# Optimization experiments

Measured on AMD Instinct MI355X. Metric: run time of the kernel, lower is better.

Reference implementation:

```python
import jax, jax.numpy as jnp
import numpy as np

D_MODEL = 1024
D_HIDDEN = 32   # per-head MPS bond dimension
N_HEADS = 8
D_FF = 4096
EPS_LN = 1e-5
EPS_NORM = 1e-6


def layernorm(x, g, b):
    m = jnp.mean(x, axis=-1, keepdims=True)
    v = jnp.mean(jnp.square(x - m), axis=-1, keepdims=True)
    return (x - m) * jax.lax.rsqrt(v + EPS_LN) * g + b


def mps_recurrence(x, Wa, ba, h0, Wo, bo):
    # x: [B,S,D]. Per-token per-head transfer matrices A_t in R^{dh x dh}.
    B, S, D = x.shape
    A = (x @ Wa + ba).reshape(B, S, N_HEADS, D_HIDDEN, D_HIDDEN)
    A = jnp.moveaxis(A, 1, 0)  # [S,B,H,dh,dh]
    h_init = jnp.broadcast_to(h0, (B, N_HEADS, D_HIDDEN))  # [B,H,dh]

    def step(h, A_t):
        h = jnp.einsum('bhij,bhj->bhi', A_t, h)
        h = h / (jnp.linalg.norm(h, axis=-1, keepdims=True) + EPS_NORM)
        return h, h

    _, ys = jax.lax.scan(step, h_init, A)          # ys: [S,B,H,dh]
    ys = jnp.moveaxis(ys, 0, 1).reshape(B, S, N_HEADS * D_HIDDEN)
    return ys @ Wo + bo                            # [B,S,D]


def setup_inputs() -> dict:
    key = jax.random.key(0)
    ks = jax.random.split(key, 12)
    B, S, D = 4, 2048, D_MODEL
    inv = 1.0 / np.sqrt(D)
    inv_hd = 1.0 / np.sqrt(N_HEADS * D_HIDDEN)
    return {
        'x': jax.random.normal(ks[0], (B, S, D), jnp.float32),
        'ln1_g': jnp.ones((D,), jnp.float32),
        'ln1_b': jnp.zeros((D,), jnp.float32),
        'Wa': jax.random.normal(ks[1], (D, N_HEADS * D_HIDDEN * D_HIDDEN), jnp.float32) * inv,
        'ba': jnp.zeros((N_HEADS * D_HIDDEN * D_HIDDEN,), jnp.float32),
        'h0': jax.random.normal(ks[2], (N_HEADS, D_HIDDEN), jnp.float32) / np.sqrt(D_HIDDEN),
        'Wo': jax.random.normal(ks[3], (N_HEADS * D_HIDDEN, D), jnp.float32) * inv_hd,
        'bo': jnp.zeros((D,), jnp.float32),
        'ln2_g': jnp.ones((D,), jnp.float32),
        'ln2_b': jnp.zeros((D,), jnp.float32),
        'W1': jax.random.normal(ks[4], (D, D_FF), jnp.float32) * inv,
        'b1': jnp.zeros((D_FF,), jnp.float32),
        'W2': jax.random.normal(ks[5], (D_FF, D), jnp.float32) / np.sqrt(D_FF),
        'b2': jnp.zeros((D,), jnp.float32),
    }


def reference(x, ln1_g, ln1_b, Wa, ba, h0, Wo, bo, ln2_g, ln2_b, W1, b1, W2, b2):
    # Dropout in eval mode (identity).
    x = x + mps_recurrence(layernorm(x, ln1_g, ln1_b), Wa, ba, h0, Wo, bo)
    h = layernorm(x, ln2_g, ln2_b)
    ffn = jax.nn.gelu(h @ W1 + b1, approximate=False) @ W2 + b2
    return x + ffn
```

## Files before the change

### kernel.cpp

```cpp
#include <hip/hip_runtime.h>
#include <hip/hip_bf16.h>
#include <math.h>

typedef float f32x4 __attribute__((ext_vector_type(4)));
typedef __bf16 bf16x4 __attribute__((ext_vector_type(4)));
typedef __bf16 bf16x8 __attribute__((ext_vector_type(8)));

#define AS1(p) ((const __attribute__((address_space(1))) void*)(p))
#define AS3(p) ((__attribute__((address_space(3))) void*)(p))

static constexpr int D_MODEL = 1024;
static constexpr int S_LEN   = 2048;
static constexpr int BATCH   = 4;
static constexpr int NTOK    = BATCH * S_LEN;
static constexpr int NH      = 8;
static constexpr int DH      = 32;
static constexpr int NA      = NH * DH * DH;
static constexpr int D_FF    = 4096;
static constexpr int CHUNK   = 16;
static constexpr int NCHUNK  = S_LEN / CHUNK;

__device__ __forceinline__ void xcd_swizzle(int& bx, int& by) {
  int gx = gridDim.x;
  int orig = by * gx + bx;
  int r8 = orig & 7, j = orig >> 3;
  int bxn = j % gx, grp = j / gx;
  bx = bxn;
  by = grp * 8 + r8;
}

__device__ __forceinline__ float gelu_erf_fast(float v) {
  float z = fabsf(v) * 0.70710678118654752f;
  float t = __builtin_amdgcn_rcpf(fmaf(0.3275911f, z, 1.0f));
  float p = t * (0.254829592f + t * (-0.284496736f + t * (1.421413741f +
            t * (-1.453152027f + t * 1.061405429f))));
  float e = __builtin_amdgcn_exp2f(-1.4426950408889634f * z * z);
  float er = 1.0f - p * e;
  er = (v < 0.0f) ? -er : er;
  return 0.5f * v * (1.0f + er);
}

__global__ __launch_bounds__(256) void transpose_bf16(
    const float* __restrict__ in, __bf16* __restrict__ out, int R, int C) {
  __shared__ float tile[32][33];
  int tx = threadIdx.x & 31, ty = threadIdx.x >> 5;
  int c0 = blockIdx.x * 32, r0 = blockIdx.y * 32;
  for (int i = ty; i < 32; i += 8)
    tile[i][tx] = in[(size_t)(r0 + i) * C + c0 + tx];
  __syncthreads();
  for (int i = ty; i < 32; i += 8)
    out[(size_t)(c0 + i) * R + r0 + tx] = (__bf16)tile[tx][i];
}

__global__ __launch_bounds__(256) void transpose_split(
    const float* __restrict__ in, __bf16* __restrict__ ohi,
    __bf16* __restrict__ olo, int R, int C) {
  __shared__ float tile[32][33];
  int tx = threadIdx.x & 31, ty = threadIdx.x >> 5;
  int c0 = blockIdx.x * 32, r0 = blockIdx.y * 32;
  for (int i = ty; i < 32; i += 8)
    tile[i][tx] = in[(size_t)(r0 + i) * C + c0 + tx];
  __syncthreads();
  for (int i = ty; i < 32; i += 8) {
    float v = tile[tx][i];
    __bf16 h = (__bf16)v;
    ohi[(size_t)(c0 + i) * R + r0 + tx] = h;
    olo[(size_t)(c0 + i) * R + r0 + tx] = (__bf16)(v - (float)h);
  }
}

template <int MODE>
__global__ __launch_bounds__(256) void ln_kernel(
    const float* __restrict__ in, const float* __restrict__ g,
    const float* __restrict__ bta, void* __restrict__ outv,
    void* __restrict__ outv2) {
  int row = blockIdx.x, tid = threadIdx.x;
  const float4* in4 = (const float4*)(in + (size_t)row * D_MODEL);
  float4 v = in4[tid];
  float s  = v.x + v.y + v.z + v.w;
  float ss = v.x * v.x + v.y * v.y + v.z * v.z + v.w * v.w;
  for (int o = 32; o; o >>= 1) { s += __shfl_down(s, o); ss += __shfl_down(ss, o); }
  __shared__ float ps[4], pq[4];
  int lane = tid & 63, w = tid >> 6;
  if (lane == 0) { ps[w] = s; pq[w] = ss; }
  __syncthreads();
  s  = ps[0] + ps[1] + ps[2] + ps[3];
  ss = pq[0] + pq[1] + pq[2] + pq[3];
  float mean = s * (1.0f / D_MODEL);
  float var  = ss * (1.0f / D_MODEL) - mean * mean;
  float inv  = rsqrtf(fmaxf(var, 0.0f) + 1e-5f);
  float4 gv = ((const float4*)g)[tid];
  float4 bv = ((const float4*)bta)[tid];
  float o0 = (v.x - mean) * inv * gv.x + bv.x;
  float o1 = (v.y - mean) * inv * gv.y + bv.y;
  float o2 = (v.z - mean) * inv * gv.z + bv.z;
  float o3 = (v.w - mean) * inv * gv.w + bv.w;
  if (MODE == 1) {
    float4 o = {o0, o1, o2, o3};
    ((float4*)outv)[(size_t)row * (D_MODEL / 4) + tid] = o;
  } else if (MODE == 0) {
    bf16x4 o;
    o[0] = (__bf16)o0; o[1] = (__bf16)o1; o[2] = (__bf16)o2; o[3] = (__bf16)o3;
    ((bf16x4*)outv)[(size_t)row * (D_MODEL / 4) + tid] = o;
  } else {
    bf16x4 oh, ol;
    oh[0] = (__bf16)o0; oh[1] = (__bf16)o1; oh[2] = (__bf16)o2; oh[3] = (__bf16)o3;
    ol[0] = (__bf16)(o0 - (float)oh[0]);
    ol[1] = (__bf16)(o1 - (float)oh[1]);
    ol[2] = (__bf16)(o2 - (float)oh[2]);
    ol[3] = (__bf16)(o3 - (float)oh[3]);
    ((bf16x4*)outv )[(size_t)row * (D_MODEL / 4) + tid] = oh;
    ((bf16x4*)outv2)[(size_t)row * (D_MODEL / 4) + tid] = ol;
  }
}

enum { EPI_BF16_BIAS = 0, EPI_BF16_BIAS_GELU = 1, EPI_F32_BIAS_RES = 2,
       EPI_F32_BIAS_ONLY = 3 };

#define PH_SYNC()                                      \
  do {                                                 \
    __builtin_amdgcn_sched_barrier(0);                 \
    __builtin_amdgcn_s_barrier();                      \
    __builtin_amdgcn_sched_barrier(0);                 \
  } while (0)
#define LGKM0()                                        \
  do {                                                 \
    asm volatile("s_waitcnt lgkmcnt(0)" ::: "memory"); \
    __builtin_amdgcn_sched_barrier(0);                 \
  } while (0)
#define GEMM8_QUAD(I0, J0)                                                   \
  do {                                                                       \
    __builtin_amdgcn_s_setprio(1);                                           \
    _Pragma("unroll") for (int i_ = 0; i_ < 4; ++i_)                         \
    _Pragma("unroll") for (int j_ = 0; j_ < 2; ++j_)                         \
    _Pragma("unroll") for (int k_ = 0; k_ < 2; ++k_)                         \
      acc[(I0) + i_][(J0) + j_] = __builtin_amdgcn_mfma_f32_16x16x32_bf16(   \
          a[(I0) + i_][k_], b[(J0) + j_][k_], acc[(I0) + i_][(J0) + j_],     \
          0, 0, 0);                                                          \
    __builtin_amdgcn_s_setprio(0);                                           \
  } while (0)

template <int SPLIT, int EPI>
__global__ __launch_bounds__(512, 2) void gemm8(
    const __bf16* __restrict__ pA, const __bf16* __restrict__ pA2,
    const __bf16* __restrict__ pB, const __bf16* __restrict__ pB2,
    const float* __restrict__ bias, void* __restrict__ out,
    int M, int N, int K) {
  __shared__ alignas(16) char lds[131072];
  const int tid = threadIdx.x;
  const int lane = tid & 63, w = tid >> 6;
  const int fm = lane & 15, fq = lane >> 4;
  const int wm2 = w >> 2, wn4 = w & 3;
  int bx = blockIdx.x, by = blockIdx.y;
  xcd_swizzle(bx, by);
  const int m0 = by * 256, n0 = bx * 256;
  const int NT = SPLIT ? 48 : (K >> 6);
  const int KS = SPLIT ? D_MODEL : K;

  const int lrow8 = lane >> 3;
  const int lslot = ((lane & 7) ^ lrow8) << 3;

  auto stageA = [&](int kt, int h) {
    const __bf16* base = SPLIT ? ((kt < 32) ? pA : pA2) : pA;
    int kc = SPLIT ? ((kt & 15) << 6) : (kt << 6);
    char* d0 = lds + ((kt & 1) << 15);
#pragma unroll
    for (int j = 0; j < 2; ++j) {
      int rb = h * 128 + j * 64 + w * 8;
      const __bf16* src = base + (size_t)(m0 + rb + lrow8) * KS + kc + lslot;
      __builtin_amdgcn_global_load_lds(AS1(src), AS3(d0 + rb * 128 + lane * 16), 16, 0, 0);
    }
  };
  auto stageB = [&](int kt, int h) {
    const __bf16* base = SPLIT ? ((kt >= 16 && kt < 32) ? pB2 : pB) : pB;
    int kc = SPLIT ? ((kt & 15) << 6) : (kt << 6);
    char* d0 = lds + 65536 + ((kt & 1) << 15);
#pragma unroll
    for (int j = 0; j < 2; ++j) {
      int rb = h * 128 + j * 64 + w * 8;
      const __bf16* src = base + (size_t)(n0 + rb + lrow8) * KS + kc + lslot;
      __builtin_amdgcn_global_load_lds(AS1(src), AS3(d0 + rb * 128 + lane * 16), 16, 0, 0);
    }
  };
  auto rdA = [&](int bo, int i, int ks) -> bf16x8 {
    int row = wm2 * 128 + i * 16 + fm;
    return *(const bf16x8*)(lds + bo + row * 128 +
                            ((((ks << 2) + fq) ^ (row & 7)) << 4));
  };
  auto rdB = [&](int bo, int j, int ks) -> bf16x8 {
    int row = wn4 * 64 + j * 16 + fm;
    return *(const bf16x8*)(lds + 65536 + bo + row * 128 +
                            ((((ks << 2) + fq) ^ (row & 7)) << 4));
  };

  f32x4 acc[8][4];
#pragma unroll
  for (int i = 0; i < 8; ++i)
#pragma unroll
    for (int j = 0; j < 4; ++j)
#pragma unroll
      for (int r = 0; r < 4; ++r) acc[i][j][r] = 0.0f;

  stageA(0, 0); stageA(0, 1); stageB(0, 0); stageB(0, 1);
  if (NT > 1) { stageA(1, 0); stageA(1, 1); }
  __builtin_amdgcn_sched_barrier(0);
  if (NT > 1) asm volatile("s_waitcnt vmcnt(4)" ::: "memory");
  else        asm volatile("s_waitcnt vmcnt(0)" ::: "memory");
  PH_SYNC();

  for (int t = 0; t < NT; ++t) {
    const int bo = (t & 1) << 15;
    bf16x8 a[8][2], b[4][2];
#pragma unroll
    for (int i = 0; i < 4; ++i) { a[i][0] = rdA(bo, i, 0); a[i][1] = rdA(bo, i, 1); }
#pragma unroll
    for (int j = 0; j < 2; ++j) { b[j][0] = rdB(bo, j, 0); b[j][1] = rdB(bo, j, 1); }
    if (t + 1 < NT) stageB(t + 1, 0);
    PH_SYNC();
    LGKM0();
    GEMM8_QUAD(0, 0);
    PH_SYNC();
#pragma unroll
    for (int j = 2; j < 4; ++j) { b[j][0] = rdB(bo, j, 0); b[j][1] = rdB(bo, j, 1); }
    if (t + 1 < NT) stageB(t + 1, 1);
    PH_SYNC();
    LGKM0();
    GEMM8_QUAD(0, 2);
    PH_SYNC();
#pragma unroll
    for (int i = 4; i < 8; ++i) { a[i][0] = rdA(bo, i, 0); a[i][1] = rdA(bo, i, 1); }
    PH_SYNC();
    LGKM0();
    GEMM8_QUAD(4, 0);
    PH_SYNC();
    if (t + 2 < NT) { stageA(t + 2, 0); stageA(t + 2, 1); }
    PH_SYNC();
    GEMM8_QUAD(4, 2);
    __builtin_amdgcn_sched_barrier(0);
    if (t + 2 < NT)
      asm volatile("s_waitcnt vmcnt(4)" ::: "memory");
    else if (t + 1 < NT)
      asm volatile("s_waitcnt vmcnt(0)" ::: "memory");
    PH_SYNC();
  }

  if (EPI == EPI_F32_BIAS_ONLY) {
    float* outF = (float*)out;
#pragma unroll
    for (int j = 0; j < 4; ++j) {
      int col = n0 + wn4 * 64 + j * 16 + fm;
      float bv = bias[col];
#pragma unroll
      for (int i = 0; i < 8; ++i)
#pragma unroll
        for (int r = 0; r < 4; ++r) {
          int row = m0 + wm2 * 128 + i * 16 + fq * 4 + r;
          outF[(size_t)row * N + col] = acc[i][j][r] + bv;
        }
    }
  } else {
    char* patch = lds + w * 16384;
    float bv4[4];
#pragma unroll
    for (int j = 0; j < 4; ++j) bv4[j] = bias[n0 + wn4 * 64 + j * 16 + fm];
#pragma unroll
    for (int i = 0; i < 8; ++i)
#pragma unroll
      for (int j = 0; j < 4; ++j)
#pragma unroll
        for (int r = 0; r < 4; ++r) {
          float v = gelu_erf_fast(acc[i][j][r] + bv4[j]);
          *(__bf16*)(patch + (i * 16 + fq * 4 + r) * 128 + (j * 16 + fm) * 2) =
              (__bf16)v;
        }
    asm volatile("s_waitcnt lgkmcnt(0)" ::: "memory");
#pragma unroll
    for (int rr = 0; rr < 16; ++rr) {
      bf16x8 ov = *(const bf16x8*)(patch + (rr * 8 + lrow8) * 128 + (lane & 7) * 16);
      size_t grow = (size_t)(m0 + wm2 * 128 + rr * 8 + lrow8);
      *(bf16x8*)((__bf16*)out + grow * N + n0 + wn4 * 64 + (lane & 7) * 8) = ov;
    }
  }
}

template <int EPI>
__global__ __launch_bounds__(256) void gemm_bf16(
    const __bf16* __restrict__ Amat, const __bf16* __restrict__ BT,
    const float* __restrict__ bias, const float* __restrict__ res,
    void* __restrict__ out, int M, int N, int K) {
  __shared__ __bf16 smem[2 * 128 * 32];
  __bf16* As = smem;
  __bf16* Bs = smem + 128 * 32;
  const int tid = threadIdx.x;
  const int lane = tid & 63, w = tid >> 6;
  int bx = blockIdx.x, by = blockIdx.y;
  xcd_swizzle(bx, by);
  const int m0 = by * 128, n0 = bx * 128;
  const int wm = (w >> 1) * 64, wn = (w & 1) * 64;

  f32x4 acc[4][4];
#pragma unroll
  for (int a = 0; a < 4; a++)
#pragma unroll
    for (int b = 0; b < 4; b++)
#pragma unroll
      for (int r = 0; r < 4; r++) acc[a][b][r] = 0.0f;

  const int srow = tid >> 2;
  const int soff = (tid & 3) * 16;
  const __bf16* gA0 = Amat + (size_t)(m0 + srow) * K + (soff >> 1);
  const __bf16* gA1 = Amat + (size_t)(m0 + srow + 64) * K + (soff >> 1);
  const __bf16* gB0 = BT + (size_t)(n0 + srow) * K + (soff >> 1);
  const __bf16* gB1 = BT + (size_t)(n0 + srow + 64) * K + (soff >> 1);
  char* lA0 = (char*)As + srow * 64 + soff;
  char* lA1 = (char*)As + (srow + 64) * 64 + soff;
  char* lB0 = (char*)Bs + srow * 64 + soff;
  char* lB1 = (char*)Bs + (srow + 64) * 64 + soff;

  const int fm = lane & 15, fq = lane >> 4;
  for (int k0 = 0; k0 < K; k0 += 32) {
    __builtin_amdgcn_global_load_lds(AS1(gA0 + k0), AS3(lA0), 16, 0, 0);
    __builtin_amdgcn_global_load_lds(AS1(gA1 + k0), AS3(lA1), 16, 0, 0);
    __builtin_amdgcn_global_load_lds(AS1(gB0 + k0), AS3(lB0), 16, 0, 0);
    __builtin_amdgcn_global_load_lds(AS1(gB1 + k0), AS3(lB1), 16, 0, 0);
    __syncthreads();
    bf16x8 af[4], bf[4];
#pragma unroll
    for (int t = 0; t < 4; t++)
      af[t] = *(const bf16x8*)((const char*)As + (wm + t * 16 + fm) * 64 + fq * 16);
#pragma unroll
    for (int t = 0; t < 4; t++)
      bf[t] = *(const bf16x8*)((const char*)Bs + (wn + t * 16 + fm) * 64 + fq * 16);
#pragma unroll
    for (int tm = 0; tm < 4; tm++)
#pragma unroll
      for (int tn = 0; tn < 4; tn++)
        acc[tm][tn] = __builtin_amdgcn_mfma_f32_16x16x32_bf16(af[tm], bf[tn], acc[tm][tn], 0, 0, 0);
    __syncthreads();
  }

#pragma unroll
  for (int tn = 0; tn < 4; tn++) {
    int col = n0 + wn + tn * 16 + fm;
    float bv = bias[col];
#pragma unroll
    for (int tm = 0; tm < 4; tm++) {
#pragma unroll
      for (int r = 0; r < 4; r++) {
        int row = m0 + wm + tm * 16 + fq * 4 + r;
        float v = acc[tm][tn][r] + bv;
        size_t idx = (size_t)row * N + col;
        if (EPI == EPI_F32_BIAS_RES) {
          ((float*)out)[idx] = v + res[idx];
        } else if (EPI == EPI_BF16_BIAS_GELU) {
          v = gelu_erf_fast(v);
          ((__bf16*)out)[idx] = (__bf16)v;
        } else {
          ((__bf16*)out)[idx] = (__bf16)v;
        }
      }
    }
  }
}

__global__ __launch_bounds__(64) void mps_chunkprod_f32(
    float* __restrict__ A) {
  int bid = blockIdx.x;
  int c = bid & 127, hh = bid >> 7;
  int lane = threadIdx.x;
  int jj = lane & 31, half = lane >> 5;
  __shared__ float Albuf[2][DH * DH];

  float curc[32];
#pragma unroll
  for (int k = 0; k < 32; k++) curc[k] = (k == jj) ? 1.0f : 0.0f;

  float* Abase = A + (size_t)(c * CHUNK) * NA + (size_t)hh * (DH * DH);

  {
    const float4* src = (const float4*)Abase;
    float4* dst = (float4*)Albuf[0];
#pragma unroll
    for (int r = 0; r < 4; r++) dst[lane + 64 * r] = src[lane + 64 * r];
  }
  __syncthreads();

  for (int t = 0; t < CHUNK; t++) {
    int cb = t & 1;
    float4 pf[4];
    if (t + 1 < CHUNK) {
      const float4* srcn = (const float4*)(Abase + (size_t)(t + 1) * NA);
#pragma unroll
      for (int r = 0; r < 4; r++) pf[r] = srcn[lane + 64 * r];
    }
    float nxt[16];
#pragma unroll
    for (int i16 = 0; i16 < 16; i16++) {
      const float4* ap = (const float4*)&Albuf[cb][(half * 16 + i16) * 32];
      float a0 = 0.f, a1 = 0.f, a2 = 0.f, a3 = 0.f;
#pragma unroll
      for (int k4 = 0; k4 < 8; k4++) {
        float4 av = ap[k4];
        a0 += av.x * curc[k4 * 4 + 0];
        a1 += av.y * curc[k4 * 4 + 1];
        a2 += av.z * curc[k4 * 4 + 2];
        a3 += av.w * curc[k4 * 4 + 3];
      }
      nxt[i16] = (a0 + a1) + (a2 + a3);
    }
    {
      float* slot = Abase + (size_t)t * NA;
#pragma unroll
      for (int i16 = 0; i16 < 16; i16++)
        slot[(half * 16 + i16) * 32 + jj] = nxt[i16];
    }
#pragma unroll
    for (int i16 = 0; i16 < 16; i16++) {
      float mine  = nxt[i16];
      float other = __shfl_xor(mine, 32);
      curc[i16]      = (half == 0) ? mine  : other;
      curc[16 + i16] = (half == 0) ? other : mine;
    }
    if (t + 1 < CHUNK) {
      float4* dst = (float4*)Albuf[cb ^ 1];
#pragma unroll
      for (int r = 0; r < 4; r++) dst[lane + 64 * r] = pf[r];
      __syncthreads();
    }
  }
}

__global__ __launch_bounds__(64) void mps_chunkscan(
    const float* __restrict__ pref, const float* __restrict__ h0,
    float* __restrict__ hstart) {
  int hh = blockIdx.x;
  int lane = threadIdx.x, i = lane & 31, half = lane >> 5;
  float hv = h0[hh * 32 + i];
  const size_t cstride = (size_t)CHUNK * NA;
  const float* row = pref + (size_t)(CHUNK - 1) * NA + (size_t)hh * (DH * DH)
                     + i * 32 + half * 16;
  int kb = half * 16;

  float4 pf0[4], pf1[4];
#pragma unroll
  for (int r = 0; r < 4; r++) pf0[r] = ((const float4*)row)[r];
#pragma unroll
  for (int r = 0; r < 4; r++) pf1[r] = ((const float4*)(row + cstride))[r];

  for (int c = 0; c < NCHUNK; c++) {
    if (lane < 32) hstart[((size_t)hh * NCHUNK + c) * 32 + i] = hv;
    float4 cur[4];
#pragma unroll
    for (int r = 0; r < 4; r++) cur[r] = pf0[r];
#pragma unroll
    for (int r = 0; r < 4; r++) pf0[r] = pf1[r];
    int cn = (c + 2 < NCHUNK) ? (c + 2) : (NCHUNK - 1);
#pragma unroll
    for (int r = 0; r < 4; r++)
      pf1[r] = ((const float4*)(row + (size_t)cn * cstride))[r];

    float a0 = 0.f, a1 = 0.f, a2 = 0.f, a3 = 0.f;
#pragma unroll
    for (int j4 = 0; j4 < 4; j4++) {
      float4 pv = cur[j4];
      a0 += pv.x * __shfl(hv, kb + j4 * 4 + 0);
      a1 += pv.y * __shfl(hv, kb + j4 * 4 + 1);
      a2 += pv.z * __shfl(hv, kb + j4 * 4 + 2);
      a3 += pv.w * __shfl(hv, kb + j4 * 4 + 3);
    }
    float y = (a0 + a1) + (a2 + a3);
    y += __shfl_xor(y, 32);
    float nn = y * y;
#pragma unroll
    for (int o = 16; o; o >>= 1) nn += __shfl_xor(nn, o);
    hv = y / (sqrtf(nn) + 1e-6f);
  }
}

__global__ __launch_bounds__(256) void mps_expand_par(
    const float* __restrict__ pref, const float* __restrict__ hstart,
    __bf16* __restrict__ ys, int tok0base) {
  int w = threadIdx.x >> 6, lane = threadIdx.x & 63;
  int i = lane & 31, half = lane >> 5;
  int task = blockIdx.x * 4 + w;
  int hh = task & 7, tok = task >> 3;
  int c = tok >> 4;
  int kb = half * 16;

  float hv = hstart[((size_t)hh * NCHUNK + c) * 32 + i];
  const float4* Mr = (const float4*)(pref + (size_t)tok * NA
                     + (size_t)hh * (DH * DH) + i * 32 + half * 16);
  float4 m0 = Mr[0], m1 = Mr[1], m2 = Mr[2], m3 = Mr[3];

  float a0 = 0.f, a1 = 0.f, a2 = 0.f, a3 = 0.f;
  a0 += m0.x * __shfl(hv, kb + 0);  a1 += m0.y * __shfl(hv, kb + 1);
  a2 += m0.z * __shfl(hv, kb + 2);  a3 += m0.w * __shfl(hv, kb + 3);
  a0 += m1.x * __shfl(hv, kb + 4);  a1 += m1.y * __shfl(hv, kb + 5);
  a2 += m1.z * __shfl(hv, kb + 6);  a3 += m1.w * __shfl(hv, kb + 7);
  a0 += m2.x * __shfl(hv, kb + 8);  a1 += m2.y * __shfl(hv, kb + 9);
  a2 += m2.z * __shfl(hv, kb + 10); a3 += m2.w * __shfl(hv, kb + 11);
  a0 += m3.x * __shfl(hv, kb + 12); a1 += m3.y * __shfl(hv, kb + 13);
  a2 += m3.z * __shfl(hv, kb + 14); a3 += m3.w * __shfl(hv, kb + 15);
  float y = (a0 + a1) + (a2 + a3);
  y += __shfl_xor(y, 32);
  float nn = y * y;
#pragma unroll
  for (int o = 16; o; o >>= 1) nn += __shfl_xor(nn, o);
  float hvo = y / (sqrtf(nn) + 1e-6f);
  if (lane < 32)
    ys[(size_t)(tok0base + tok) * (NH * DH) + hh * 32 + i] = (__bf16)hvo;
}

extern "C" void kernel_launch(void* const* d_in, const int* in_sizes, int n_in,
                              void* d_out, int out_size, void* d_ws, size_t ws_size,
                              hipStream_t stream) {
  const float* x     = (const float*)d_in[0];
  const float* ln1_g = (const float*)d_in[1];
  const float* ln1_b = (const float*)d_in[2];
  const float* Wa    = (const float*)d_in[3];
  const float* ba    = (const float*)d_in[4];
  const float* h0    = (const float*)d_in[5];
  const float* Wo    = (const float*)d_in[6];
  const float* bo    = (const float*)d_in[7];
  const float* ln2_g = (const float*)d_in[8];
  const float* ln2_b = (const float*)d_in[9];
  const float* W1    = (const float*)d_in[10];
  const float* b1    = (const float*)d_in[11];
  const float* W2    = (const float*)d_in[12];
  const float* b2    = (const float*)d_in[13];
  float* out = (float*)d_out;

  char* wsb = (char*)d_ws;
  size_t off = 0;
  auto alloc = [&](size_t bytes) -> void* {
    void* p = wsb + off;
    off += (bytes + 255) & ~(size_t)255;
    return p;
  };
  __bf16* WoT   = (__bf16*)alloc((size_t)(NH * DH) * D_MODEL * 2);
  __bf16* W1T   = (__bf16*)alloc((size_t)D_MODEL * D_FF * 2);
  __bf16* W2T   = (__bf16*)alloc((size_t)D_FF * D_MODEL * 2);
  __bf16* ys    = (__bf16*)alloc((size_t)NTOK * NH * DH * 2);
  float*  hst   = (float*) alloc((size_t)NH * NCHUNK * DH * 4);
  __bf16* xnh   = (__bf16*)alloc((size_t)NTOK * D_MODEL * 2);
  __bf16* xnl   = (__bf16*)alloc((size_t)NTOK * D_MODEL * 2);
  __bf16* WaTh  = (__bf16*)alloc((size_t)D_MODEL * NA * 2);
  __bf16* WaTl  = (__bf16*)alloc((size_t)D_MODEL * NA * 2);
  size_t tail0 = off;
  float*  Af32 = (float*) alloc((size_t)S_LEN * NA * 4);
  __bf16* mid  = (__bf16*)(wsb + tail0);

  transpose_bf16<<<dim3(D_MODEL / 32, (NH * DH) / 32), 256, 0, stream>>>(Wo, WoT, NH * DH, D_MODEL);
  transpose_bf16<<<dim3(D_FF / 32, D_MODEL / 32), 256, 0, stream>>>(W1, W1T, D_MODEL, D_FF);
  transpose_bf16<<<dim3(D_MODEL / 32, D_FF / 32), 256, 0, stream>>>(W2, W2T, D_FF, D_MODEL);
  transpose_split<<<dim3(NA / 32, D_MODEL / 32), 256, 0, stream>>>(Wa, WaTh, WaTl, D_MODEL, NA);

  ln_kernel<2><<<NTOK, 256, 0, stream>>>(x, ln1_g, ln1_b, xnh, xnl);

  for (int b = 0; b < BATCH; b++) {
    gemm8<1, EPI_F32_BIAS_ONLY><<<dim3(NA / 256, S_LEN / 256), 512, 0, stream>>>(
        xnh + (size_t)b * S_LEN * D_MODEL, xnl + (size_t)b * S_LEN * D_MODEL,
        WaTh, WaTl, ba, Af32, S_LEN, NA, D_MODEL);
    mps_chunkprod_f32<<<NH * NCHUNK, 64, 0, stream>>>(Af32);
    mps_chunkscan<<<NH, 64, 0, stream>>>(Af32, h0, hst);
    mps_expand_par<<<(S_LEN * NH) / 4, 256, 0, stream>>>(Af32, hst, ys, b * S_LEN);
  }

  gemm_bf16<EPI_F32_BIAS_RES><<<dim3(D_MODEL / 128, NTOK / 128), 256, 0, stream>>>(
      ys, WoT, bo, x, out, NTOK, D_MODEL, NH * DH);

  ln_kernel<0><<<NTOK, 256, 0, stream>>>(out, ln2_g, ln2_b, xnh, nullptr);

  gemm8<0, EPI_BF16_BIAS_GELU><<<dim3(D_FF / 256, NTOK / 256), 512, 0, stream>>>(
      xnh, nullptr, W1T, nullptr, b1, mid, NTOK, D_FF, D_MODEL);

  gemm_bf16<EPI_F32_BIAS_RES><<<dim3(D_MODEL / 128, NTOK / 128), 256, 0, stream>>>(
      mid, W2T, b2, out, out, NTOK, D_MODEL, D_FF);
}
```

Baseline: 1.473 ms.

## Restructure GEMM main loop to overlap LDS reads with MFMA and prefetch next tile

Reschedules the bf16 GEMM inner loop so that LDS fragment reads for the next quadrant are issued before the current quadrant's MFMAs, and the first fragments of the next K-tile are loaded during the last MFMA quadrant. Global-to-LDS staging is reordered (stageA halves split across iterations, waits reduced to vmcnt(2)), and fragment registers are hoisted out of the loop. The aim is to hide LDS latency and cut the number of barriers per iteration. In exchange it keeps more fragments live in registers and makes the buffer hazards subtler.

```diff
diff --git a/kernel.cpp b/kernel.cpp
--- a/kernel.cpp
+++ b/kernel.cpp
@@ -117,16 +117,17 @@
 enum { EPI_BF16_BIAS = 0, EPI_BF16_BIAS_GELU = 1, EPI_F32_BIAS_RES = 2,
        EPI_F32_BIAS_ONLY = 3 };
 
-#define PH_SYNC()                                      \
+#define SB0() __builtin_amdgcn_sched_barrier(0)
+#define BARRIER()                                      \
   do {                                                 \
-    __builtin_amdgcn_sched_barrier(0);                 \
+    SB0();                                             \
     __builtin_amdgcn_s_barrier();                      \
-    __builtin_amdgcn_sched_barrier(0);                 \
+    SB0();                                             \
   } while (0)
 #define LGKM0()                                        \
   do {                                                 \
     asm volatile("s_waitcnt lgkmcnt(0)" ::: "memory"); \
-    __builtin_amdgcn_sched_barrier(0);                 \
+    SB0();                                             \
   } while (0)
 #define GEMM8_QUAD(I0, J0)                                                   \
   do {                                                                       \
@@ -202,47 +203,53 @@
       for (int r = 0; r < 4; ++r) acc[i][j][r] = 0.0f;
 
   stageA(0, 0); stageA(0, 1); stageB(0, 0); stageB(0, 1);
-  if (NT > 1) { stageA(1, 0); stageA(1, 1); }
-  __builtin_amdgcn_sched_barrier(0);
-  if (NT > 1) asm volatile("s_waitcnt vmcnt(4)" ::: "memory");
+  if (NT > 1) stageA(1, 0);
+  SB0();
+  if (NT > 1) asm volatile("s_waitcnt vmcnt(2)" ::: "memory");
   else        asm volatile("s_waitcnt vmcnt(0)" ::: "memory");
-  PH_SYNC();
+  BARRIER();
+  bf16x8 a[8][2], b[4][2];
+#pragma unroll
+  for (int i = 0; i < 4; ++i) { a[i][0] = rdA(0, i, 0); a[i][1] = rdA(0, i, 1); }
+#pragma unroll
+  for (int j = 0; j < 2; ++j) { b[j][0] = rdB(0, j, 0); b[j][1] = rdB(0, j, 1); }
 
   for (int t = 0; t < NT; ++t) {
-    const int bo = (t & 1) << 15;
-    bf16x8 a[8][2], b[4][2];
-#pragma unroll
-    for (int i = 0; i < 4; ++i) { a[i][0] = rdA(bo, i, 0); a[i][1] = rdA(bo, i, 1); }
-#pragma unroll
-    for (int j = 0; j < 2; ++j) { b[j][0] = rdB(bo, j, 0); b[j][1] = rdB(bo, j, 1); }
-    if (t + 1 < NT) stageB(t + 1, 0);
-    PH_SYNC();
+    const int bo  = (t & 1) << 15;
+    const int bon = ((t + 1) & 1) << 15;
+    BARRIER();
+    if (t + 1 < NT) { stageA(t + 1, 1); stageB(t + 1, 0); }
     LGKM0();
+#pragma unroll
+    for (int j = 2; j < 4; ++j) { b[j][0] = rdB(bo, j, 0); b[j][1] = rdB(bo, j, 1); }
+    SB0();
     GEMM8_QUAD(0, 0);
-    PH_SYNC();
-#pragma unroll
-    for (int j = 2; j < 4; ++j) { b[j][0] = rdB(bo, j, 0); b[j][1] = rdB(bo, j, 1); }
+    BARRIER();
     if (t + 1 < NT) stageB(t + 1, 1);
-    PH_SYNC();
     LGKM0();
+#pragma unroll
+    for (int i = 4; i < 8; ++i) { a[i][0] = rdA(bo, i, 0); a[i][1] = rdA(bo, i, 1); }
+    SB0();
     GEMM8_QUAD(0, 2);
-    PH_SYNC();
-#pragma unroll
-    for (int i = 4; i < 8; ++i) { a[i][0] = rdA(bo, i, 0); a[i][1] = rdA(bo, i, 1); }
-    PH_SYNC();
+    BARRIER();
     LGKM0();
     GEMM8_QUAD(4, 0);
-    PH_SYNC();
-    if (t + 2 < NT) { stageA(t + 2, 0); stageA(t + 2, 1); }
-    PH_SYNC();
+    BARRIER();
+    if (t + 2 < NT) stageA(t + 2, 0);
+    SB0();
+    if (t + 1 < NT) {
+      if (t + 2 < NT) asm volatile("s_waitcnt vmcnt(2)" ::: "memory");
+      else            asm volatile("s_waitcnt vmcnt(0)" ::: "memory");
+      BARRIER();
+#pragma unroll
+      for (int i = 0; i < 4; ++i) { a[i][0] = rdA(bon, i, 0); a[i][1] = rdA(bon, i, 1); }
+#pragma unroll
+      for (int j = 0; j < 2; ++j) { b[j][0] = rdB(bon, j, 0); b[j][1] = rdB(bon, j, 1); }
+      SB0();
+    }
     GEMM8_QUAD(4, 2);
-    __builtin_amdgcn_sched_barrier(0);
-    if (t + 2 < NT)
-      asm volatile("s_waitcnt vmcnt(4)" ::: "memory");
-    else if (t + 1 < NT)
-      asm volatile("s_waitcnt vmcnt(0)" ::: "memory");
-    PH_SYNC();
-  }
+  }
+  __syncthreads();
 
   if (EPI == EPI_F32_BIAS_ONLY) {
     float* outF = (float*)out;
```

New measurement: 1.452 ms. No clear change (-1.4%).
